# Kernel optimization log

Hardware: AMD Instinct MI355X
Metric: run time of the kernel (lower is better)

The kernel has to match this reference:

```python
import jax, jax.numpy as jnp
import numpy as np

D_MODEL = 1024
NUM_HEADS = 16
DEPTH = D_MODEL // NUM_HEADS


def setup_inputs() -> dict:
    key = jax.random.key(0)
    ks = jax.random.split(key, 11)
    B, S = 4, 2048
    scale = 1.0 / np.sqrt(D_MODEL)
    inp = {
        "query": jax.random.normal(ks[0], (B, S, D_MODEL), jnp.float32),
        "key": jax.random.normal(ks[1], (B, S, D_MODEL), jnp.float32),
        "value": jax.random.normal(ks[2], (B, S, D_MODEL), jnp.float32),
        # Linear params (torch nn.Linear: y = x @ W.T + b); store W as [out, in]
        "wq_w": jax.random.normal(ks[3], (D_MODEL, D_MODEL), jnp.float32) * scale,
        "wq_b": jnp.zeros((D_MODEL,), jnp.float32),
        "wk_w": jax.random.normal(ks[4], (D_MODEL, D_MODEL), jnp.float32) * scale,
        "wk_b": jnp.zeros((D_MODEL,), jnp.float32),
        "wv_w": jax.random.normal(ks[5], (D_MODEL, D_MODEL), jnp.float32) * scale,
        "wv_b": jnp.zeros((D_MODEL,), jnp.float32),
        "dense_w": jax.random.normal(ks[6], (D_MODEL, D_MODEL), jnp.float32) * scale,
        "dense_b": jnp.zeros((D_MODEL,), jnp.float32),
    }
    return inp


def _split_heads(x, B):
    # [B, S, D] -> [B, H, S, depth]
    return x.reshape(B, -1, NUM_HEADS, DEPTH).transpose(0, 2, 1, 3)


def reference(query, key, value, wq_w, wq_b, wk_w, wk_b, wv_w, wv_b, dense_w, dense_b):
    B = query.shape[0]
    q = _split_heads(query @ wq_w.T + wq_b, B)   # [B,H,Sq,depth]
    k = _split_heads(key @ wk_w.T + wk_b, B)     # [B,H,Sk,depth]
    v = _split_heads(value @ wv_w.T + wv_b, B)   # [B,H,Sk,depth]
    scores = jnp.einsum("bhqd,bhkd->bhqk", q, k) / jnp.sqrt(jnp.float32(DEPTH)).astype(q.dtype)
    attn = jax.nn.softmax(scores, axis=-1)
    out = jnp.einsum("bhqk,bhkd->bhqd", attn, v)  # [B,H,Sq,depth]
    out = out.transpose(0, 2, 1, 3).reshape(B, -1, D_MODEL)
    return out @ dense_w.T + dense_b
```

## Files before the change

kernel.cpp:

```cpp
#include <hip/hip_runtime.h>
#include <hip/hip_bf16.h>
#include <stdint.h>


#define SEQ    2048
#define DEPTH  64
#define HEADS  16
#define NMODEL 1024
#define MROWS  8192

typedef __bf16 bf16x8 __attribute__((ext_vector_type(8)));
typedef float  f32x4  __attribute__((ext_vector_type(4)));

__device__ __forceinline__ unsigned short f32_bf16(float f) {
    union { float f; unsigned int u; } c; c.f = f;
    unsigned int u = c.u + 0x7FFFu + ((c.u >> 16) & 1u);
    return (unsigned short)(u >> 16);
}

__device__ __forceinline__ void gload16(const unsigned short* g, unsigned short* l) {
    __builtin_amdgcn_global_load_lds(
        (const __attribute__((address_space(1))) unsigned int*)g,
        (__attribute__((address_space(3))) unsigned int*)l, 16, 0, 0);
}

__global__ __launch_bounds__(256) void cvt3_kernel(
    const float* __restrict__ a, const float* __restrict__ b, const float* __restrict__ c,
    unsigned short* __restrict__ oa, unsigned short* __restrict__ ob,
    unsigned short* __restrict__ oc, int n4)
{
    const float* in; unsigned short* out;
    if (blockIdx.y == 0) { in = a; out = oa; }
    else if (blockIdx.y == 1) { in = b; out = ob; }
    else { in = c; out = oc; }
    int i = blockIdx.x * 256 + threadIdx.x;
    if (i < n4) {
        float4 f = ((const float4*)in)[i];
        ushort4 o;
        o.x = f32_bf16(f.x); o.y = f32_bf16(f.y);
        o.z = f32_bf16(f.z); o.w = f32_bf16(f.w);
        ((ushort4*)out)[i] = o;
    }
}

__global__ __launch_bounds__(256) void cvt4_kernel(
    const float* __restrict__ a, const float* __restrict__ b,
    const float* __restrict__ c, const float* __restrict__ d,
    unsigned short* __restrict__ oa, unsigned short* __restrict__ ob,
    unsigned short* __restrict__ oc, unsigned short* __restrict__ od, int n4)
{
    const float* in; unsigned short* out;
    if (blockIdx.y == 0) { in = a; out = oa; }
    else if (blockIdx.y == 1) { in = b; out = ob; }
    else if (blockIdx.y == 2) { in = c; out = oc; }
    else { in = d; out = od; }
    int i = blockIdx.x * 256 + threadIdx.x;
    if (i < n4) {
        float4 f = ((const float4*)in)[i];
        ushort4 o;
        o.x = f32_bf16(f.x); o.y = f32_bf16(f.y);
        o.z = f32_bf16(f.z); o.w = f32_bf16(f.w);
        ((ushort4*)out)[i] = o;
    }
}

__device__ __forceinline__ void gemm128_core(
    const unsigned short* __restrict__ A, const unsigned short* __restrict__ W,
    const float* __restrict__ bias, void* __restrict__ outp,
    int mode, float scale, int m0, int n0,
    unsigned short* Alds, unsigned short* Blds)
{
    const int tid  = threadIdx.x;
    const int wave = tid >> 6, lane = tid & 63;
    const int l15  = lane & 15, quad = lane >> 4;
    const int wm   = wave & 1,  wn   = wave >> 1;
    const int swz  = l15 & 7;
    const int K    = 1024;

    f32x4 acc[4][4] = {};

    const int lrow = lane >> 3;
    const int fcol = ((lane & 7) ^ lrow) << 3;
    const unsigned short* Ab[4];
    const unsigned short* Bb[4];
    #pragma unroll
    for (int c = 0; c < 4; ++c) {
        const int seg = 4 * wave + c;
        Ab[c] = A + (size_t)(m0 + seg * 8 + lrow) * K + fcol;
        Bb[c] = W + (size_t)(n0 + seg * 8 + lrow) * K + fcol;
    }

    for (int k0 = 0; k0 < K; k0 += 64) {
        #pragma unroll
        for (int c = 0; c < 4; ++c) {
            gload16(Ab[c] + k0, &Alds[(4 * wave + c) * 512]);
            gload16(Bb[c] + k0, &Blds[(4 * wave + c) * 512]);
        }
        __syncthreads();

        #pragma unroll
        for (int kc = 0; kc < 2; ++kc) {
            bf16x8 a[4], b[4];
            const int pg = (((kc * 4 + quad) ^ swz) << 3);
            #pragma unroll
            for (int i = 0; i < 4; ++i)
                a[i] = *(const bf16x8*)&Alds[(wm * 64 + i * 16 + l15) * 64 + pg];
            #pragma unroll
            for (int j = 0; j < 4; ++j)
                b[j] = *(const bf16x8*)&Blds[(wn * 64 + j * 16 + l15) * 64 + pg];
            #pragma unroll
            for (int i = 0; i < 4; ++i)
                #pragma unroll
                for (int j = 0; j < 4; ++j)
                    acc[i][j] = __builtin_amdgcn_mfma_f32_16x16x32_bf16(a[i], b[j], acc[i][j], 0, 0, 0);
        }
        __syncthreads();
    }

    #pragma unroll
    for (int i = 0; i < 4; ++i) {
        #pragma unroll
        for (int j = 0; j < 4; ++j) {
            const int col = n0 + wn * 64 + j * 16 + l15;
            const int row_b = m0 + wm * 64 + i * 16 + quad * 4;
            if (mode == 2) {
                const int colp = (col & ~31)
                               | (col & 3)
                               | (((col >> 4) & 1) << 2)
                               | (((col >> 2) & 3) << 3);
                #pragma unroll
                for (int r = 0; r < 4; ++r) {
                    const int row = row_b + r;
                    ((unsigned short*)outp)[(size_t)row * MROWS + colp] =
                        f32_bf16(acc[i][j][r] + bias[row]);
                }
            } else if (mode == 0) {
                const float bv = bias[col];
                #pragma unroll
                for (int r = 0; r < 4; ++r)
                    ((float*)outp)[(size_t)(row_b + r) * NMODEL + col] = acc[i][j][r] + bv;
            } else {
                const float bv = bias[col];
                const int h_ = col >> 6, d_ = col & 63;
                #pragma unroll
                for (int r = 0; r < 4; ++r) {
                    const int row = row_b + r;
                    const int b_ = row >> 11, s_ = row & 2047;
                    ((unsigned short*)outp)[(((size_t)(b_ * HEADS + h_) * SEQ + s_) << 6) + d_] =
                        f32_bf16((acc[i][j][r] + bv) * scale);
                }
            }
        }
    }
}

__global__ __launch_bounds__(256, 3) void gemm_qkv(
    const unsigned short* __restrict__ qb,  const unsigned short* __restrict__ wqb,
    const float* __restrict__ bq, unsigned short* __restrict__ Qp,
    const unsigned short* __restrict__ kb,  const unsigned short* __restrict__ wkb,
    const float* __restrict__ bk, unsigned short* __restrict__ Kpj,
    const unsigned short* __restrict__ wvb, const unsigned short* __restrict__ vb,
    const float* __restrict__ bv, unsigned short* __restrict__ Vtg,
    float qscale)
{
    __shared__ unsigned short Alds[128 * 64];
    __shared__ unsigned short Blds[128 * 64];
    const int bid = blockIdx.x, z = blockIdx.y;
    if (z == 0) {
        gemm128_core(qb, wqb, bq, Qp, 1, qscale, (bid >> 3) * 128, (bid & 7) * 128, Alds, Blds);
    } else if (z == 1) {
        gemm128_core(kb, wkb, bk, Kpj, 1, 1.0f, (bid >> 3) * 128, (bid & 7) * 128, Alds, Blds);
    } else {
        gemm128_core(wvb, vb, bv, Vtg, 2, 1.0f, (bid & 7) * 128, (bid >> 3) * 128, Alds, Blds);
    }
}

__global__ __launch_bounds__(256, 3) void gemm_dense(
    const unsigned short* __restrict__ A, const unsigned short* __restrict__ W,
    const float* __restrict__ bias, float* __restrict__ out)
{
    __shared__ unsigned short Alds[128 * 64];
    __shared__ unsigned short Blds[128 * 64];
    const int bid = blockIdx.x;
    gemm128_core(A, W, bias, out, 0, 1.0f, (bid >> 3) * 128, (bid & 7) * 128, Alds, Blds);
}

__global__ __launch_bounds__(256, 2) void attn_fwd(
    const unsigned short* __restrict__ Qp,
    const unsigned short* __restrict__ Kp,
    const unsigned short* __restrict__ Vtg,
    unsigned short* __restrict__ Op)
{
    __shared__ unsigned short Klds[2 * 64 * 64];
    __shared__ unsigned short Vlds[2 * 64 * 64];
    const int tid  = threadIdx.x;
    const int wave = tid >> 6, lane = tid & 63;
    const int l15  = lane & 15, quad = lane >> 4;
    const int swz  = l15 & 7;
    const int bh   = blockIdx.y;
    const int b_   = bh >> 4, h_ = bh & 15;
    const int q0   = blockIdx.x * 256;

    const unsigned short* Qb = Qp + (size_t)bh * SEQ * DEPTH;
    const unsigned short* Kb = Kp + (size_t)bh * SEQ * DEPTH;
    const unsigned short* Vb = Vtg + (size_t)h_ * DEPTH * MROWS + (size_t)b_ * SEQ;

    const int srow = (wave << 3) + (lane >> 3);
    const int scg  = (lane & 7) ^ ((lane >> 3) & 7);

    const unsigned short* Kg0 = Kb + (size_t)srow * DEPTH + scg * 8;
    const unsigned short* Kg1 = Kb + (size_t)(srow + 32) * DEPTH + scg * 8;
    const unsigned short* Vg0 = Vb + (size_t)srow * MROWS + scg * 8;
    const unsigned short* Vg1 = Vb + (size_t)(srow + 32) * MROWS + scg * 8;

    bf16x8 qf[4][2];
    #pragma unroll
    for (int i = 0; i < 4; ++i)
        #pragma unroll
        for (int kc = 0; kc < 2; ++kc)
            qf[i][kc] = *(const bf16x8*)(Qb + (size_t)(q0 + wave * 64 + i * 16 + l15) * DEPTH
                                         + kc * 32 + quad * 8);

    union { bf16x8 v; unsigned short s[8]; } uo;
    #pragma unroll
    for (int j = 0; j < 8; ++j) uo.s[j] = 0x3F80;
    const bf16x8 ones = uo.v;

    f32x4 Ot[4][4] = {};
    f32x4 lacc[4]  = {};

    auto STAGE = [&](int buf, int kt) {
        unsigned short* KW = &Klds[buf * 4096 + wave * 512];
        unsigned short* VW = &Vlds[buf * 4096 + wave * 512];
        gload16(Kg0 + (size_t)kt * 4096, KW);
        gload16(Kg1 + (size_t)kt * 4096, KW + 2048);
        gload16(Vg0 + kt * 64, VW);
        gload16(Vg1 + kt * 64, VW + 2048);
    };

    STAGE(0, 0);
    asm volatile("s_waitcnt vmcnt(0)" ::: "memory");
    __builtin_amdgcn_s_barrier();

    for (int kt = 0; kt < SEQ / 64; ++kt) {
        const int cur = kt & 1;
        if (kt + 1 < SEQ / 64) STAGE(cur ^ 1, kt + 1);

        const unsigned short* Kc = &Klds[cur * 4096];

        #pragma unroll
        for (int half = 0; half < 2; ++half) {
            __builtin_amdgcn_s_setprio(1);
            const int r0 = (2 * half) * 16 + l15;
            const int r1 = (2 * half + 1) * 16 + l15;
            bf16x8 ka0 = *(const bf16x8*)&Kc[r0 * 64 + ((quad ^ swz) << 3)];
            bf16x8 ka1 = *(const bf16x8*)&Kc[r0 * 64 + (((4 + quad) ^ swz) << 3)];
            bf16x8 kb0 = *(const bf16x8*)&Kc[r1 * 64 + ((quad ^ swz) << 3)];
            bf16x8 kb1 = *(const bf16x8*)&Kc[r1 * 64 + (((4 + quad) ^ swz) << 3)];
            f32x4 S0[4], S1[4];
            #pragma unroll
            for (int i = 0; i < 4; ++i) {
                S0[i] = f32x4{};
                S0[i] = __builtin_amdgcn_mfma_f32_16x16x32_bf16(ka0, qf[i][0], S0[i], 0, 0, 0);
                S0[i] = __builtin_amdgcn_mfma_f32_16x16x32_bf16(ka1, qf[i][1], S0[i], 0, 0, 0);
                S1[i] = f32x4{};
                S1[i] = __builtin_amdgcn_mfma_f32_16x16x32_bf16(kb0, qf[i][0], S1[i], 0, 0, 0);
                S1[i] = __builtin_amdgcn_mfma_f32_16x16x32_bf16(kb1, qf[i][1], S1[i], 0, 0, 0);
            }
            __builtin_amdgcn_s_setprio(0);

            bf16x8 pfh[4];
            #pragma unroll
            for (int i = 0; i < 4; ++i) {
                float e0 = __builtin_amdgcn_exp2f(S0[i][0]);
                float e1 = __builtin_amdgcn_exp2f(S0[i][1]);
                float e2 = __builtin_amdgcn_exp2f(S0[i][2]);
                float e3 = __builtin_amdgcn_exp2f(S0[i][3]);
                float e4 = __builtin_amdgcn_exp2f(S1[i][0]);
                float e5 = __builtin_amdgcn_exp2f(S1[i][1]);
                float e6 = __builtin_amdgcn_exp2f(S1[i][2]);
                float e7 = __builtin_amdgcn_exp2f(S1[i][3]);
                union { bf16x8 v; __hip_bfloat162 h[4]; } up;
                up.h[0] = __float22bfloat162_rn(make_float2(e0, e1));
                up.h[1] = __float22bfloat162_rn(make_float2(e2, e3));
                up.h[2] = __float22bfloat162_rn(make_float2(e4, e5));
                up.h[3] = __float22bfloat162_rn(make_float2(e6, e7));
                pfh[i] = up.v;
            }

            __builtin_amdgcn_s_setprio(1);
            lacc[0] = __builtin_amdgcn_mfma_f32_16x16x32_bf16(ones, pfh[0], lacc[0], 0, 0, 0);
            lacc[1] = __builtin_amdgcn_mfma_f32_16x16x32_bf16(ones, pfh[1], lacc[1], 0, 0, 0);
            lacc[2] = __builtin_amdgcn_mfma_f32_16x16x32_bf16(ones, pfh[2], lacc[2], 0, 0, 0);
            lacc[3] = __builtin_amdgcn_mfma_f32_16x16x32_bf16(ones, pfh[3], lacc[3], 0, 0, 0);
            #pragma unroll
            for (int dd = 0; dd < 4; ++dd) {
                bf16x8 vf = *(const bf16x8*)&Vlds[cur * 4096 +
                            (dd * 16 + l15) * 64 + (((half * 4 + quad) ^ swz) << 3)];
                #pragma unroll
                for (int i = 0; i < 4; ++i)
                    Ot[i][dd] = __builtin_amdgcn_mfma_f32_16x16x32_bf16(vf, pfh[i], Ot[i][dd], 0, 0, 0);
            }
            __builtin_amdgcn_s_setprio(0);
        }

        asm volatile("s_waitcnt vmcnt(0)" ::: "memory");
        __builtin_amdgcn_s_barrier();
    }

    #pragma unroll
    for (int i = 0; i < 4; ++i) {
        const float inv = 1.0f / lacc[i][0];
        const int row = b_ * SEQ + q0 + wave * 64 + i * 16 + l15;
        #pragma unroll
        for (int dd = 0; dd < 4; ++dd) {
            ushort4 ov;
            ov.x = f32_bf16(Ot[i][dd][0] * inv);
            ov.y = f32_bf16(Ot[i][dd][1] * inv);
            ov.z = f32_bf16(Ot[i][dd][2] * inv);
            ov.w = f32_bf16(Ot[i][dd][3] * inv);
            const int col = h_ * 64 + dd * 16 + quad * 4;
            *(ushort4*)&Op[(size_t)row * NMODEL + col] = ov;
        }
    }
}

extern "C" void kernel_launch(void* const* d_in, const int* in_sizes, int n_in,
                              void* d_out, int out_size, void* d_ws, size_t ws_size,
                              hipStream_t stream) {
    const float* q  = (const float*)d_in[0];
    const float* k  = (const float*)d_in[1];
    const float* v  = (const float*)d_in[2];
    const float* wq = (const float*)d_in[3];
    const float* bq = (const float*)d_in[4];
    const float* wk = (const float*)d_in[5];
    const float* bk = (const float*)d_in[6];
    const float* wv = (const float*)d_in[7];
    const float* bv = (const float*)d_in[8];
    const float* wd = (const float*)d_in[9];
    const float* bd = (const float*)d_in[10];

    char* ws = (char*)d_ws;
    size_t off = 0;
    auto alloc = [&](size_t bytes) { char* p = ws + off; off += bytes; return p; };
    const size_t ACT = (size_t)MROWS * NMODEL * 2;
    const size_t WGT = (size_t)NMODEL * NMODEL * 2;

    unsigned short* qb   = (unsigned short*)alloc(ACT);
    unsigned short* kb   = (unsigned short*)alloc(ACT);
    unsigned short* vb   = (unsigned short*)alloc(ACT);
    unsigned short* wqb  = (unsigned short*)alloc(WGT);
    unsigned short* wkb  = (unsigned short*)alloc(WGT);
    unsigned short* wvb  = (unsigned short*)alloc(WGT);
    unsigned short* wdb  = (unsigned short*)alloc(WGT);
    unsigned short* Qp   = (unsigned short*)alloc(ACT);
    unsigned short* Kpj  = (unsigned short*)alloc(ACT);
    unsigned short* Vtg  = (unsigned short*)alloc(ACT);
    unsigned short* attn = (unsigned short*)alloc(ACT);

    const int nAct4 = MROWS * NMODEL / 4;
    const int nWgt4 = NMODEL * NMODEL / 4;
    cvt3_kernel<<<dim3(nAct4 / 256, 3), 256, 0, stream>>>(q, k, v, qb, kb, vb, nAct4);
    cvt4_kernel<<<dim3(nWgt4 / 256, 4), 256, 0, stream>>>(wq, wk, wv, wd,
                                                          wqb, wkb, wvb, wdb, nWgt4);

    const float SC = 0.18033688011112042f;
    gemm_qkv<<<dim3(512, 3), 256, 0, stream>>>(qb, wqb, bq, Qp,
                                               kb, wkb, bk, Kpj,
                                               wvb, vb, bv, Vtg, SC);

    attn_fwd<<<dim3(SEQ / 256, 64), 256, 0, stream>>>(Qp, Kpj, Vtg, attn);

    gemm_dense<<<512, 256, 0, stream>>>(attn, wdb, bd, (float*)d_out);
}
```

Baseline: 321.3 us.

## Rewrite projection GEMMs as 256x128 double-buffered 8-wave tiles with prefetch

The projection and dense GEMMs move from a 128x128 tile with 4 waves and a single LDS buffer to a 256x128 tile with 8 waves and double-buffered LDS. The next k-tile is prefetched with global_load_lds while MFMAs run, and s_setprio is raised around the MFMA bursts. Block IDs are remapped so that consecutive blocks share weight columns for better L2 reuse. This aims to hide global-load latency and cut barrier stalls, at the cost of more LDS per block (96 KB), fewer blocks, and more barriers per k-step.

```diff
diff --git a/kernel.cpp b/kernel.cpp
--- a/kernel.cpp
+++ b/kernel.cpp
@@ -64,65 +64,132 @@
     }
 }
 
-__device__ __forceinline__ void gemm128_core(
+__device__ __forceinline__ void gemm256_core(
     const unsigned short* __restrict__ A, const unsigned short* __restrict__ W,
     const float* __restrict__ bias, void* __restrict__ outp,
     int mode, float scale, int m0, int n0,
-    unsigned short* Alds, unsigned short* Blds)
+    unsigned short* __restrict__ Alds, unsigned short* __restrict__ Blds)
 {
     const int tid  = threadIdx.x;
     const int wave = tid >> 6, lane = tid & 63;
     const int l15  = lane & 15, quad = lane >> 4;
-    const int wm   = wave & 1,  wn   = wave >> 1;
+    const int wr   = wave >> 1, wc = wave & 1;
     const int swz  = l15 & 7;
     const int K    = 1024;
 
     f32x4 acc[4][4] = {};
 
-    const int lrow = lane >> 3;
-    const int fcol = ((lane & 7) ^ lrow) << 3;
-    const unsigned short* Ab[4];
-    const unsigned short* Bb[4];
+    const int trow = tid >> 3;
+    const int tg   = ((tid & 7) ^ (trow & 7)) << 3;
+    const unsigned short* Asrc[2][2];
+    const unsigned short* Bsrc[2];
     #pragma unroll
-    for (int c = 0; c < 4; ++c) {
-        const int seg = 4 * wave + c;
-        Ab[c] = A + (size_t)(m0 + seg * 8 + lrow) * K + fcol;
-        Bb[c] = W + (size_t)(n0 + seg * 8 + lrow) * K + fcol;
-    }
-
-    for (int k0 = 0; k0 < K; k0 += 64) {
+    for (int u = 0; u < 2; ++u) {
         #pragma unroll
-        for (int c = 0; c < 4; ++c) {
-            gload16(Ab[c] + k0, &Alds[(4 * wave + c) * 512]);
-            gload16(Bb[c] + k0, &Blds[(4 * wave + c) * 512]);
-        }
-        __syncthreads();
-
-        #pragma unroll
-        for (int kc = 0; kc < 2; ++kc) {
-            bf16x8 a[4], b[4];
-            const int pg = (((kc * 4 + quad) ^ swz) << 3);
-            #pragma unroll
-            for (int i = 0; i < 4; ++i)
-                a[i] = *(const bf16x8*)&Alds[(wm * 64 + i * 16 + l15) * 64 + pg];
-            #pragma unroll
-            for (int j = 0; j < 4; ++j)
-                b[j] = *(const bf16x8*)&Blds[(wn * 64 + j * 16 + l15) * 64 + pg];
-            #pragma unroll
-            for (int i = 0; i < 4; ++i)
-                #pragma unroll
-                for (int j = 0; j < 4; ++j)
-                    acc[i][j] = __builtin_amdgcn_mfma_f32_16x16x32_bf16(a[i], b[j], acc[i][j], 0, 0, 0);
-        }
-        __syncthreads();
+        for (int s = 0; s < 2; ++s)
+            Asrc[u][s] = A + (size_t)(m0 + u * 128 + s * 64 + trow) * K + tg;
+        Bsrc[u] = W + (size_t)(n0 + u * 64 + trow) * K + tg;
+    }
+
+    auto STAGE = [&](int buf, int kt2, int u) {
+        gload16(Asrc[u][0] + kt2 * 64, Alds + buf * 16384 + (u * 128 + wave * 8) * 64);
+        gload16(Asrc[u][1] + kt2 * 64, Alds + buf * 16384 + (u * 128 + 64 + wave * 8) * 64);
+        gload16(Bsrc[u]    + kt2 * 64, Blds + buf * 8192  + (u * 64 + wave * 8) * 64);
+    };
+
+    STAGE(0, 0, 0);
+    STAGE(0, 0, 1);
+    asm volatile("s_waitcnt vmcnt(0)" ::: "memory");
+    __builtin_amdgcn_s_barrier();
+
+    for (int kt = 0; kt < 16; ++kt) {
+        const int cur = kt & 1;
+        const unsigned short* Ab = Alds + cur * 16384;
+        const unsigned short* Bb = Blds + cur * 8192;
+        const int arow = wr * 64 + l15;
+        const int brow = wc * 64 + l15;
+        const bool pre = (kt + 1 < 16);
+        bf16x8 bfr[4], af0, af1;
+
+        {
+            const int pg = ((quad ^ swz) << 3);
+            bfr[0] = *(const bf16x8*)&Bb[(brow)      * 64 + pg];
+            bfr[1] = *(const bf16x8*)&Bb[(brow + 16) * 64 + pg];
+            bfr[2] = *(const bf16x8*)&Bb[(brow + 32) * 64 + pg];
+            bfr[3] = *(const bf16x8*)&Bb[(brow + 48) * 64 + pg];
+            af0    = *(const bf16x8*)&Ab[(arow)      * 64 + pg];
+            af1    = *(const bf16x8*)&Ab[(arow + 16) * 64 + pg];
+            if (pre) STAGE(cur ^ 1, kt + 1, 0);
+            __builtin_amdgcn_s_barrier();
+            __builtin_amdgcn_s_setprio(1);
+            #pragma unroll
+            for (int j = 0; j < 4; ++j)
+                acc[0][j] = __builtin_amdgcn_mfma_f32_16x16x32_bf16(af0, bfr[j], acc[0][j], 0, 0, 0);
+            #pragma unroll
+            for (int j = 0; j < 4; ++j)
+                acc[1][j] = __builtin_amdgcn_mfma_f32_16x16x32_bf16(af1, bfr[j], acc[1][j], 0, 0, 0);
+            __builtin_amdgcn_s_setprio(0);
+            __builtin_amdgcn_s_barrier();
+        }
+        {
+            const int pg = ((quad ^ swz) << 3);
+            af0 = *(const bf16x8*)&Ab[(arow + 32) * 64 + pg];
+            af1 = *(const bf16x8*)&Ab[(arow + 48) * 64 + pg];
+            if (pre) STAGE(cur ^ 1, kt + 1, 1);
+            __builtin_amdgcn_s_barrier();
+            __builtin_amdgcn_s_setprio(1);
+            #pragma unroll
+            for (int j = 0; j < 4; ++j)
+                acc[2][j] = __builtin_amdgcn_mfma_f32_16x16x32_bf16(af0, bfr[j], acc[2][j], 0, 0, 0);
+            #pragma unroll
+            for (int j = 0; j < 4; ++j)
+                acc[3][j] = __builtin_amdgcn_mfma_f32_16x16x32_bf16(af1, bfr[j], acc[3][j], 0, 0, 0);
+            __builtin_amdgcn_s_setprio(0);
+            __builtin_amdgcn_s_barrier();
+        }
+        {
+            const int pg = (((4 + quad) ^ swz) << 3);
+            bfr[0] = *(const bf16x8*)&Bb[(brow)      * 64 + pg];
+            bfr[1] = *(const bf16x8*)&Bb[(brow + 16) * 64 + pg];
+            bfr[2] = *(const bf16x8*)&Bb[(brow + 32) * 64 + pg];
+            bfr[3] = *(const bf16x8*)&Bb[(brow + 48) * 64 + pg];
+            af0    = *(const bf16x8*)&Ab[(arow)      * 64 + pg];
+            af1    = *(const bf16x8*)&Ab[(arow + 16) * 64 + pg];
+            __builtin_amdgcn_s_barrier();
+            __builtin_amdgcn_s_setprio(1);
+            #pragma unroll
+            for (int j = 0; j < 4; ++j)
+                acc[0][j] = __builtin_amdgcn_mfma_f32_16x16x32_bf16(af0, bfr[j], acc[0][j], 0, 0, 0);
+            #pragma unroll
+            for (int j = 0; j < 4; ++j)
+                acc[1][j] = __builtin_amdgcn_mfma_f32_16x16x32_bf16(af1, bfr[j], acc[1][j], 0, 0, 0);
+            __builtin_amdgcn_s_setprio(0);
+            __builtin_amdgcn_s_barrier();
+        }
+        {
+            const int pg = (((4 + quad) ^ swz) << 3);
+            af0 = *(const bf16x8*)&Ab[(arow + 32) * 64 + pg];
+            af1 = *(const bf16x8*)&Ab[(arow + 48) * 64 + pg];
+            __builtin_amdgcn_s_barrier();
+            __builtin_amdgcn_s_setprio(1);
+            #pragma unroll
+            for (int j = 0; j < 4; ++j)
+                acc[2][j] = __builtin_amdgcn_mfma_f32_16x16x32_bf16(af0, bfr[j], acc[2][j], 0, 0, 0);
+            #pragma unroll
+            for (int j = 0; j < 4; ++j)
+                acc[3][j] = __builtin_amdgcn_mfma_f32_16x16x32_bf16(af1, bfr[j], acc[3][j], 0, 0, 0);
+            __builtin_amdgcn_s_setprio(0);
+            asm volatile("s_waitcnt vmcnt(0)" ::: "memory");
+            __builtin_amdgcn_s_barrier();
+        }
     }
 
     #pragma unroll
     for (int i = 0; i < 4; ++i) {
         #pragma unroll
         for (int j = 0; j < 4; ++j) {
-            const int col = n0 + wn * 64 + j * 16 + l15;
-            const int row_b = m0 + wm * 64 + i * 16 + quad * 4;
+            const int col = n0 + wc * 64 + j * 16 + l15;
+            const int row_b = m0 + wr * 64 + i * 16 + quad * 4;
             if (mode == 2) {
                 const int colp = (col & ~31)
                                | (col & 3)
@@ -154,7 +221,7 @@
     }
 }
 
-__global__ __launch_bounds__(256, 3) void gemm_qkv(
+__global__ __launch_bounds__(512, 2) void gemm_qkv(
     const unsigned short* __restrict__ qb,  const unsigned short* __restrict__ wqb,
     const float* __restrict__ bq, unsigned short* __restrict__ Qp,
     const unsigned short* __restrict__ kb,  const unsigned short* __restrict__ wkb,
@@ -163,26 +230,28 @@
     const float* __restrict__ bv, unsigned short* __restrict__ Vtg,
     float qscale)
 {
-    __shared__ unsigned short Alds[128 * 64];
-    __shared__ unsigned short Blds[128 * 64];
-    const int bid = blockIdx.x, z = blockIdx.y;
+    __shared__ unsigned short Alds[2 * 256 * 64];
+    __shared__ unsigned short Blds[2 * 128 * 64];
+    const int o = blockIdx.x, z = blockIdx.y;
+    const int sid = (o & 7) * 32 + (o >> 3);
     if (z == 0) {
-        gemm128_core(qb, wqb, bq, Qp, 1, qscale, (bid >> 3) * 128, (bid & 7) * 128, Alds, Blds);
+        gemm256_core(qb, wqb, bq, Qp, 1, qscale, (sid >> 3) * 256, (sid & 7) * 128, Alds, Blds);
     } else if (z == 1) {
-        gemm128_core(kb, wkb, bk, Kpj, 1, 1.0f, (bid >> 3) * 128, (bid & 7) * 128, Alds, Blds);
+        gemm256_core(kb, wkb, bk, Kpj, 1, 1.0f, (sid >> 3) * 256, (sid & 7) * 128, Alds, Blds);
     } else {
-        gemm128_core(wvb, vb, bv, Vtg, 2, 1.0f, (bid & 7) * 128, (bid >> 3) * 128, Alds, Blds);
-    }
-}
-
-__global__ __launch_bounds__(256, 3) void gemm_dense(
+        gemm256_core(wvb, vb, bv, Vtg, 2, 1.0f, (sid & 3) * 256, (sid >> 2) * 128, Alds, Blds);
+    }
+}
+
+__global__ __launch_bounds__(512, 2) void gemm_dense(
     const unsigned short* __restrict__ A, const unsigned short* __restrict__ W,
     const float* __restrict__ bias, float* __restrict__ out)
 {
-    __shared__ unsigned short Alds[128 * 64];
-    __shared__ unsigned short Blds[128 * 64];
-    const int bid = blockIdx.x;
-    gemm128_core(A, W, bias, out, 0, 1.0f, (bid >> 3) * 128, (bid & 7) * 128, Alds, Blds);
+    __shared__ unsigned short Alds[2 * 256 * 64];
+    __shared__ unsigned short Blds[2 * 128 * 64];
+    const int o = blockIdx.x;
+    const int sid = (o & 7) * 32 + (o >> 3);
+    gemm256_core(A, W, bias, out, 0, 1.0f, (sid >> 3) * 256, (sid & 7) * 128, Alds, Blds);
 }
 
 __global__ __launch_bounds__(256, 2) void attn_fwd(
@@ -365,11 +434,11 @@
                                                           wqb, wkb, wvb, wdb, nWgt4);
 
     const float SC = 0.18033688011112042f;
-    gemm_qkv<<<dim3(512, 3), 256, 0, stream>>>(qb, wqb, bq, Qp,
+    gemm_qkv<<<dim3(256, 3), 512, 0, stream>>>(qb, wqb, bq, Qp,
                                                kb, wkb, bk, Kpj,
                                                wvb, vb, bv, Vtg, SC);
 
     attn_fwd<<<dim3(SEQ / 256, 64), 256, 0, stream>>>(Qp, Kpj, Vtg, attn);
 
-    gemm_dense<<<512, 256, 0, stream>>>(attn, wdb, bd, (float*)d_out);
-}
+    gemm_dense<<<256, 512, 0, stream>>>(attn, wdb, bd, (float*)d_out);
+}
```

After: 330.6 us. +2.9%, slower.
